# Performance work log

Measured on AMD Instinct MI355X. Metric: run time of the kernel, lower is better.

The kernel has to match this reference:

```python
import jax, jax.numpy as jnp
import numpy as np

EMBED_DIM = 1024
NUM_HEADS = 16
HEAD_DIM = EMBED_DIM // NUM_HEADS


def setup_inputs() -> dict:
    key = jax.random.key(0)
    k_x, k_qkv, k_proj, k_pb = jax.random.split(key, 4)
    B, N = 8, 1024
    s = 1.0 / np.sqrt(EMBED_DIM)
    return {
        "x": jax.random.normal(k_x, (B, N, EMBED_DIM), dtype=jnp.float32),
        # qkv: Linear(embed_dim -> 3*all_head_dim), bias=False
        "w_qkv": jax.random.uniform(k_qkv, (EMBED_DIM, 3 * EMBED_DIM), dtype=jnp.float32, minval=-s, maxval=s),
        # proj: Linear(all_head_dim -> embed_dim), with bias
        "w_proj": jax.random.uniform(k_proj, (EMBED_DIM, EMBED_DIM), dtype=jnp.float32, minval=-s, maxval=s),
        "b_proj": jax.random.uniform(k_pb, (EMBED_DIM,), dtype=jnp.float32, minval=-s, maxval=s),
    }


def reference(x, w_qkv, w_proj, b_proj):
    B, N, _ = x.shape
    scale = HEAD_DIM ** -0.5
    qkv = jnp.einsum("bnd,de->bne", x, w_qkv)  # [B, N, 3*D]
    q, k, v = jnp.split(qkv, 3, axis=-1)
    # reshape to heads: [B, H, N, hd]
    def heads(t):
        return t.reshape(B, N, NUM_HEADS, HEAD_DIM).transpose(0, 2, 1, 3)
    q, k, v = heads(q), heads(k), heads(v)
    attn = jnp.einsum("bhqd,bhkd->bhqk", q, k) * scale
    attn = jax.nn.softmax(attn, axis=-1)
    out = jnp.einsum("bhqk,bhkd->bhqd", attn, v)
    out = out.transpose(0, 2, 1, 3).reshape(B, N, NUM_HEADS * HEAD_DIM)
    return jnp.einsum("bnd,de->bne", out, w_proj) + b_proj
```

## Files before the change

kernel.cpp:

```cpp
#include <hip/hip_runtime.h>
#include <hip/hip_bf16.h>
#include <stdint.h>

typedef __hip_bfloat16 bf16;
typedef __attribute__((ext_vector_type(8))) __bf16 bf16x8;
typedef __attribute__((ext_vector_type(4))) float f32x4;

__device__ __forceinline__ bf16x8 load8bf(const bf16* p) {
    return __builtin_bit_cast(bf16x8, *(const int4*)p);
}

__device__ __forceinline__ void async16(const bf16* g, bf16* l) {
    __builtin_amdgcn_global_load_lds((const __attribute__((address_space(1))) void*)g,
                                     (__attribute__((address_space(3))) void*)l, 16, 0, 0);
}

__global__ __launch_bounds__(256) void cast_x_kernel(const float* __restrict__ in,
                                                     bf16* __restrict__ out, int n4) {
    int i = blockIdx.x * 256 + threadIdx.x;
    if (i >= n4) return;
    float4 v = ((const float4*)in)[i];
    ushort4 o;
    o.x = __builtin_bit_cast(unsigned short, __float2bfloat16(v.x));
    o.y = __builtin_bit_cast(unsigned short, __float2bfloat16(v.y));
    o.z = __builtin_bit_cast(unsigned short, __float2bfloat16(v.z));
    o.w = __builtin_bit_cast(unsigned short, __float2bfloat16(v.w));
    ((ushort4*)out)[i] = o;
}

__global__ __launch_bounds__(256) void transpose_cast(const float* __restrict__ in,
                                                      bf16* __restrict__ out, int R, int C) {
    __shared__ float t[32][33];
    int c0 = blockIdx.x * 32, r0 = blockIdx.y * 32;
    int tx = threadIdx.x, ty = threadIdx.y;
#pragma unroll
    for (int j = 0; j < 32; j += 8)
        t[ty + j][tx] = in[(size_t)(r0 + ty + j) * C + c0 + tx];
    __syncthreads();
#pragma unroll
    for (int j = 0; j < 32; j += 8)
        out[(size_t)(c0 + ty + j) * R + r0 + tx] = __float2bfloat16(t[tx][ty + j]);
}

template <int MODE>
__global__ __launch_bounds__(256) void gemm_bt(
    const bf16* __restrict__ A, const bf16* __restrict__ Bt,
    int M, int N, int K,
    bf16* __restrict__ qo, bf16* __restrict__ ko, bf16* __restrict__ vto,
    float* __restrict__ out, const float* __restrict__ bias) {
    __shared__ __align__(16) bf16 Al0[128 * 64];
    __shared__ __align__(16) bf16 Bl0[128 * 64];
    __shared__ __align__(16) bf16 Al1[128 * 64];
    __shared__ __align__(16) bf16 Bl1[128 * 64];
    const int tid = threadIdx.x;
    const int l = tid & 63, wid = tid >> 6;
    const int lo = l & 15, hi = l >> 4;
    const int wm = wid >> 1, wn = wid & 1;
    const int m0 = blockIdx.x * 128, n0 = blockIdx.y * 128;
    const int sr = tid >> 3;
    const int cl = (tid & 7) * 8;
    const int csw = ((tid & 7) ^ (sr & 7)) * 8;

    f32x4 acc[4][4];
#pragma unroll
    for (int i = 0; i < 4; ++i)
#pragma unroll
        for (int j = 0; j < 4; ++j) acc[i][j] = f32x4{0.f, 0.f, 0.f, 0.f};

#define STAGE_A(DST, KT)                                                              \
    _Pragma("unroll") for (int s_ = 0; s_ < 4; ++s_) {                                \
        int r_ = s_ * 32 + sr;                                                        \
        async16(A + (size_t)(m0 + r_) * K + (KT) * 64 + csw, DST + r_ * 64 + cl);     \
    }
#define STAGE_B(DST, KT)                                                              \
    _Pragma("unroll") for (int s_ = 0; s_ < 4; ++s_) {                                \
        int r_ = s_ * 32 + sr;                                                        \
        async16(Bt + (size_t)(n0 + r_) * K + (KT) * 64 + csw, DST + r_ * 64 + cl);    \
    }
#define KBODY(AL, BL, ANXT, BNXT, KT, STG)                                            \
    {                                                                                 \
        __syncthreads();        \
        if (STG) { STAGE_A(ANXT, (KT) + 1); }                                         \
        __builtin_amdgcn_sched_barrier(0);                                            \
        bf16x8 af[4][2], bfv0[2][2];                                                  \
        _Pragma("unroll") for (int mt = 0; mt < 4; ++mt) {                            \
            int ar = wm * 64 + mt * 16 + lo;                                          \
            _Pragma("unroll") for (int ks = 0; ks < 2; ++ks)                          \
                af[mt][ks] = load8bf(AL + ar * 64 + ((ks * 32 + hi * 8) ^ ((ar & 7) * 8))); \
        }                                                                             \
        _Pragma("unroll") for (int nt = 0; nt < 2; ++nt) {                            \
            int br = wn * 64 + nt * 16 + lo;                                          \
            _Pragma("unroll") for (int ks = 0; ks < 2; ++ks)                          \
                bfv0[nt][ks] = load8bf(BL + br * 64 + ((ks * 32 + hi * 8) ^ ((br & 7) * 8))); \
        }                                                                             \
        _Pragma("unroll") for (int mt = 0; mt < 4; ++mt)                              \
            _Pragma("unroll") for (int nt = 0; nt < 2; ++nt)                          \
                _Pragma("unroll") for (int ks = 0; ks < 2; ++ks)                      \
                    acc[mt][nt] = __builtin_amdgcn_mfma_f32_16x16x32_bf16(            \
                        af[mt][ks], bfv0[nt][ks], acc[mt][nt], 0, 0, 0);              \
        if (STG) { STAGE_B(BNXT, (KT) + 1); }                                         \
        __builtin_amdgcn_sched_barrier(0);                                            \
        bf16x8 bfv1[2][2];                                                            \
        _Pragma("unroll") for (int nt = 0; nt < 2; ++nt) {                            \
            int br = wn * 64 + (nt + 2) * 16 + lo;                                    \
            _Pragma("unroll") for (int ks = 0; ks < 2; ++ks)                          \
                bfv1[nt][ks] = load8bf(BL + br * 64 + ((ks * 32 + hi * 8) ^ ((br & 7) * 8))); \
        }                                                                             \
        _Pragma("unroll") for (int mt = 0; mt < 4; ++mt)                              \
            _Pragma("unroll") for (int nt = 0; nt < 2; ++nt)                          \
                _Pragma("unroll") for (int ks = 0; ks < 2; ++ks)                      \
                    acc[mt][nt + 2] = __builtin_amdgcn_mfma_f32_16x16x32_bf16(        \
                        af[mt][ks], bfv1[nt][ks], acc[mt][nt + 2], 0, 0, 0);          \
    }

    const int nkt = K / 64;
    STAGE_A(Al0, 0)
    STAGE_B(Bl0, 0)
    for (int kt = 0; kt < nkt; kt += 2) {
        KBODY(Al0, Bl0, Al1, Bl1, kt, true)
        KBODY(Al1, Bl1, Al0, Bl0, kt + 1, (kt + 2 < nkt))
    }
#undef KBODY
#undef STAGE_B
#undef STAGE_A

#pragma unroll
    for (int mt = 0; mt < 4; ++mt)
#pragma unroll
        for (int nt = 0; nt < 4; ++nt)
#pragma unroll
            for (int r = 0; r < 4; ++r) {
                int row = m0 + wm * 64 + mt * 16 + hi * 4 + r;
                int col = n0 + wn * 64 + nt * 16 + lo;
                float v = acc[mt][nt][r];
                if (MODE == 0) {
                    if (col < 1024) {
                        qo[(size_t)row * 1024 + col] = __float2bfloat16(v * 0.125f);
                    } else if (col < 2048) {
                        ko[(size_t)row * 1024 + (col - 1024)] = __float2bfloat16(v);
                    } else {
                        int c = col - 2048;
                        vto[((size_t)(row >> 10) * 1024 + c) * 1024 + (row & 1023)] = __float2bfloat16(v);
                    }
                } else {
                    out[(size_t)row * N + col] = v + bias[col];
                }
            }
}

__global__ __launch_bounds__(256, 3) void flash_attn(
    const bf16* __restrict__ q,
    const bf16* __restrict__ kin,
    const bf16* __restrict__ vt,
    bf16* __restrict__ out)
{
    __shared__ __align__(16) bf16 Kl0[64 * 64];
    __shared__ __align__(16) bf16 Vl0[64 * 64];
    __shared__ __align__(16) bf16 Kl1[64 * 64];
    __shared__ __align__(16) bf16 Vl1[64 * 64];
    __shared__ __align__(16) bf16 Pl[4 * 32 * 72];
    const int tid = threadIdx.x;
    const int l = tid & 63, w = tid >> 6;
    const int lo = l & 15, hi = l >> 4;
    const int bid = (blockIdx.x & 7) * 128 + (blockIdx.x >> 3);
    const int qt = bid & 7, h = (bid >> 3) & 15, b = bid >> 7;
    const int ts_r = tid >> 3;
    const int ts_c = tid & 7;
    const int ts_csw = (ts_c ^ (ts_r & 7)) * 8;
    const int ts_lds = tid * 8;

    const bf16* kbase = kin + (size_t)(b * 1024) * 1024 + h * 64;
    const bf16* vbase = vt + (size_t)(b * 1024 + h * 64) * 1024;

#define STAGE_KV(KD, VD, KT)                                                          \
    {                                                                                 \
        async16(kbase + (size_t)((KT) * 64 + ts_r) * 1024 + ts_csw, (KD) + ts_lds);   \
        async16(kbase + (size_t)((KT) * 64 + 32 + ts_r) * 1024 + ts_csw,              \
                (KD) + 2048 + ts_lds);                                                \
        async16(vbase + (size_t)ts_r * 1024 + (KT) * 64 + ts_csw, (VD) + ts_lds);     \
        async16(vbase + (size_t)(32 + ts_r) * 1024 + (KT) * 64 + ts_csw,              \
                (VD) + 2048 + ts_lds);                                                \
    }

    bf16x8 qf[2][2];
#pragma unroll
    for (int mt = 0; mt < 2; ++mt)
#pragma unroll
        for (int ks = 0; ks < 2; ++ks) {
            int tok = qt * 128 + w * 32 + mt * 16 + lo;
            qf[mt][ks] = load8bf(q + (size_t)(b * 1024 + tok) * 1024 + h * 64 + ks * 32 + hi * 8);
        }

    float lsum[2][4];
    f32x4 oacc[2][4];
#pragma unroll
    for (int mt = 0; mt < 2; ++mt)
#pragma unroll
        for (int r = 0; r < 4; ++r) lsum[mt][r] = 0.f;
#pragma unroll
    for (int mt = 0; mt < 2; ++mt)
#pragma unroll
        for (int nt = 0; nt < 4; ++nt) oacc[mt][nt] = f32x4{0.f, 0.f, 0.f, 0.f};

    STAGE_KV(Kl0, Vl0, 0)
    __syncthreads();

#define FA_ITER(KC, VC, KN, VN, KT, STG)                                              \
    {                                                                                 \
        if (STG) { STAGE_KV(KN, VN, (KT) + 1) }                                       \
        __builtin_amdgcn_sched_barrier(0);                                            \
        f32x4 s[2][4];                                                                \
        _Pragma("unroll") for (int mt = 0; mt < 2; ++mt)                              \
            _Pragma("unroll") for (int nt = 0; nt < 4; ++nt)                          \
                s[mt][nt] = f32x4{0.f, 0.f, 0.f, 0.f};                                \
        _Pragma("unroll") for (int ks = 0; ks < 2; ++ks) {                            \
            bf16x8 kf[4];                                                             \
            _Pragma("unroll") for (int nt = 0; nt < 4; ++nt) {                        \
                int kr = nt * 16 + lo;                                                \
                kf[nt] = load8bf((KC) + kr * 64 + ((ks * 32 + hi * 8) ^ ((kr & 7) * 8))); \
            }                                                                         \
            _Pragma("unroll") for (int mt = 0; mt < 2; ++mt)                          \
                _Pragma("unroll") for (int nt = 0; nt < 4; ++nt)                      \
                    s[mt][nt] = __builtin_amdgcn_mfma_f32_16x16x32_bf16(              \
                        qf[mt][ks], kf[nt], s[mt][nt], 0, 0, 0);                      \
        }                                                                             \
        _Pragma("unroll") for (int mt = 0; mt < 2; ++mt)                              \
            _Pragma("unroll") for (int nt = 0; nt < 4; ++nt)                          \
                _Pragma("unroll") for (int r = 0; r < 4; ++r) {                       \
                    float p = __expf(s[mt][nt][r]);                                   \
                    lsum[mt][r] += p;                                                 \
                    Pl[(w * 32 + mt * 16 + hi * 4 + r) * 72 + nt * 16 + lo] =         \
                        __float2bfloat16(p);                                          \
                }                                                                     \
        _Pragma("unroll") for (int ks = 0; ks < 2; ++ks) {                            \
            bf16x8 vf[4], pf[2];                                                      \
            _Pragma("unroll") for (int nt = 0; nt < 4; ++nt) {                        \
                int vr = nt * 16 + lo;                                                \
                vf[nt] = load8bf((VC) + vr * 64 + ((ks * 32 + hi * 8) ^ ((vr & 7) * 8))); \
            }                                                                         \
            _Pragma("unroll") for (int mt = 0; mt < 2; ++mt)                          \
                pf[mt] = load8bf(Pl + (w * 32 + mt * 16 + lo) * 72 + ks * 32 + hi * 8); \
            _Pragma("unroll") for (int mt = 0; mt < 2; ++mt)                          \
                _Pragma("unroll") for (int nt = 0; nt < 4; ++nt)                      \
                    oacc[mt][nt] = __builtin_amdgcn_mfma_f32_16x16x32_bf16(           \
                        pf[mt], vf[nt], oacc[mt][nt], 0, 0, 0);                       \
        }                                                                             \
        __syncthreads();        \
    }

    for (int kt = 0; kt < 16; kt += 2) {
        FA_ITER(Kl0, Vl0, Kl1, Vl1, kt, true)
        FA_ITER(Kl1, Vl1, Kl0, Vl0, kt + 1, (kt + 2 < 16))
    }
#undef FA_ITER
#undef STAGE_KV

#pragma unroll
    for (int mt = 0; mt < 2; ++mt)
#pragma unroll
        for (int r = 0; r < 4; ++r) {
#pragma unroll
            for (int off = 1; off < 16; off <<= 1)
                lsum[mt][r] += __shfl_xor(lsum[mt][r], off);
        }

#pragma unroll
    for (int mt = 0; mt < 2; ++mt)
#pragma unroll
        for (int nt = 0; nt < 4; ++nt)
#pragma unroll
            for (int r = 0; r < 4; ++r) {
                int tok = qt * 128 + w * 32 + mt * 16 + hi * 4 + r;
                int d = nt * 16 + lo;
                out[(size_t)(b * 1024 + tok) * 1024 + h * 64 + d] =
                    __float2bfloat16(oacc[mt][nt][r] / lsum[mt][r]);
            }
}

extern "C" void kernel_launch(void* const* d_in, const int* in_sizes, int n_in,
                              void* d_out, int out_size, void* d_ws, size_t ws_size,
                              hipStream_t stream) {
    const float* x      = (const float*)d_in[0];
    const float* w_qkv  = (const float*)d_in[1];
    const float* w_proj = (const float*)d_in[2];
    const float* b_proj = (const float*)d_in[3];
    float* out = (float*)d_out;

    char* ws = (char*)d_ws;
    bf16* xb     = (bf16*)(ws);
    bf16* wqkvT  = (bf16*)(ws + (16ull << 20));
    bf16* wprojT = (bf16*)(ws + (22ull << 20));
    bf16* qb     = (bf16*)(ws + (24ull << 20));
    bf16* kb     = (bf16*)(ws + (40ull << 20));
    bf16* vtb    = (bf16*)(ws + (56ull << 20));
    bf16* attn   = xb;

    cast_x_kernel<<<8192, 256, 0, stream>>>(x, xb, 2 * 1024 * 1024);
    transpose_cast<<<dim3(96, 32), dim3(32, 8), 0, stream>>>(w_qkv, wqkvT, 1024, 3072);
    transpose_cast<<<dim3(32, 32), dim3(32, 8), 0, stream>>>(w_proj, wprojT, 1024, 1024);
    gemm_bt<0><<<dim3(64, 24), 256, 0, stream>>>(xb, wqkvT, 8192, 3072, 1024,
                                                 qb, kb, vtb, nullptr, nullptr);
    flash_attn<<<1024, 256, 0, stream>>>(qb, kb, vtb, attn);
    gemm_bt<1><<<dim3(64, 8), 256, 0, stream>>>(attn, wprojT, 8192, 1024, 1024,
                                                nullptr, nullptr, nullptr, out, b_proj);
}
```

Measured before the change: 157.1 us.

## Triple-buffer GEMM K-loop with 32-wide tiles and explicit vmcnt waits

The GEMM mainloop moves from double-buffered 64-wide K tiles to triple-buffered 32-wide K tiles, prefetching two stages ahead. Each iteration is fenced with raw s_barrier and explicit s_waitcnt vmcnt counts, so loads can stay in flight across iterations. Shared memory per block is smaller and the kernel requests 3 blocks per CU through launch bounds, aiming for more latency hiding and higher occupancy. The tail is hard-coded for K/32 = 32 iterations, so the kernel is only correct for K=1024, and the hand-written waitcnt values have to match exactly how many async loads are outstanding.

```diff
diff --git a/kernel.cpp b/kernel.cpp
--- a/kernel.cpp
+++ b/kernel.cpp
@@ -43,23 +43,27 @@
 }
 
 template <int MODE>
-__global__ __launch_bounds__(256) void gemm_bt(
+__global__ __launch_bounds__(256, 3) void gemm_bt(
     const bf16* __restrict__ A, const bf16* __restrict__ Bt,
     int M, int N, int K,
     bf16* __restrict__ qo, bf16* __restrict__ ko, bf16* __restrict__ vto,
     float* __restrict__ out, const float* __restrict__ bias) {
-    __shared__ __align__(16) bf16 Al0[128 * 64];
-    __shared__ __align__(16) bf16 Bl0[128 * 64];
-    __shared__ __align__(16) bf16 Al1[128 * 64];
-    __shared__ __align__(16) bf16 Bl1[128 * 64];
+    __shared__ __align__(16) bf16 A0[128 * 32];
+    __shared__ __align__(16) bf16 B0[128 * 32];
+    __shared__ __align__(16) bf16 A1[128 * 32];
+    __shared__ __align__(16) bf16 B1[128 * 32];
+    __shared__ __align__(16) bf16 A2[128 * 32];
+    __shared__ __align__(16) bf16 B2[128 * 32];
     const int tid = threadIdx.x;
     const int l = tid & 63, wid = tid >> 6;
     const int lo = l & 15, hi = l >> 4;
     const int wm = wid >> 1, wn = wid & 1;
     const int m0 = blockIdx.x * 128, n0 = blockIdx.y * 128;
-    const int sr = tid >> 3;
-    const int cl = (tid & 7) * 8;
-    const int csw = ((tid & 7) ^ (sr & 7)) * 8;
+    const int tsr = tid >> 2;
+    const int tsc = tid & 3;
+    const int csw = ((tsc ^ (tsr & 3)) * 8);
+    const int cl  = tsc * 8;
+    const int colr = ((hi ^ (lo & 3)) * 8);
 
     f32x4 acc[4][4];
 #pragma unroll
@@ -67,62 +71,51 @@
 #pragma unroll
         for (int j = 0; j < 4; ++j) acc[i][j] = f32x4{0.f, 0.f, 0.f, 0.f};
 
-#define STAGE_A(DST, KT)                                                              \
-    _Pragma("unroll") for (int s_ = 0; s_ < 4; ++s_) {                                \
-        int r_ = s_ * 32 + sr;                                                        \
-        async16(A + (size_t)(m0 + r_) * K + (KT) * 64 + csw, DST + r_ * 64 + cl);     \
-    }
-#define STAGE_B(DST, KT)                                                              \
-    _Pragma("unroll") for (int s_ = 0; s_ < 4; ++s_) {                                \
-        int r_ = s_ * 32 + sr;                                                        \
-        async16(Bt + (size_t)(n0 + r_) * K + (KT) * 64 + csw, DST + r_ * 64 + cl);    \
-    }
-#define KBODY(AL, BL, ANXT, BNXT, KT, STG)                                            \
-    {                                                                                 \
-        __syncthreads();        \
-        if (STG) { STAGE_A(ANXT, (KT) + 1); }                                         \
-        __builtin_amdgcn_sched_barrier(0);                                            \
-        bf16x8 af[4][2], bfv0[2][2];                                                  \
-        _Pragma("unroll") for (int mt = 0; mt < 4; ++mt) {                            \
-            int ar = wm * 64 + mt * 16 + lo;                                          \
-            _Pragma("unroll") for (int ks = 0; ks < 2; ++ks)                          \
-                af[mt][ks] = load8bf(AL + ar * 64 + ((ks * 32 + hi * 8) ^ ((ar & 7) * 8))); \
-        }                                                                             \
-        _Pragma("unroll") for (int nt = 0; nt < 2; ++nt) {                            \
-            int br = wn * 64 + nt * 16 + lo;                                          \
-            _Pragma("unroll") for (int ks = 0; ks < 2; ++ks)                          \
-                bfv0[nt][ks] = load8bf(BL + br * 64 + ((ks * 32 + hi * 8) ^ ((br & 7) * 8))); \
-        }                                                                             \
+#define STAGE32(AD, BD, KT)                                                           \
+    {                                                                                 \
+        async16(A + (size_t)(m0 + tsr) * K + (KT) * 32 + csw, (AD) + tsr * 32 + cl);  \
+        async16(A + (size_t)(m0 + 64 + tsr) * K + (KT) * 32 + csw,                    \
+                (AD) + (64 + tsr) * 32 + cl);                                         \
+        async16(Bt + (size_t)(n0 + tsr) * K + (KT) * 32 + csw, (BD) + tsr * 32 + cl); \
+        async16(Bt + (size_t)(n0 + 64 + tsr) * K + (KT) * 32 + csw,                   \
+                (BD) + (64 + tsr) * 32 + cl);                                         \
+    }
+
+#define KB(AC, BC, AS, BS, KT, STG, WAITASM)                                          \
+    {                                                                                 \
+        __builtin_amdgcn_s_barrier();           \
+        __builtin_amdgcn_sched_barrier(0);       \
+        if (STG) STAGE32(AS, BS, (KT) + 2)                                            \
+        __builtin_amdgcn_sched_barrier(0);          \
+        asm volatile(WAITASM ::: "memory");                                           \
+        __builtin_amdgcn_s_barrier();            \
+        __builtin_amdgcn_sched_barrier(0);       \
+        bf16x8 af[4], bf_[4];                                                         \
         _Pragma("unroll") for (int mt = 0; mt < 4; ++mt)                              \
-            _Pragma("unroll") for (int nt = 0; nt < 2; ++nt)                          \
-                _Pragma("unroll") for (int ks = 0; ks < 2; ++ks)                      \
-                    acc[mt][nt] = __builtin_amdgcn_mfma_f32_16x16x32_bf16(            \
-                        af[mt][ks], bfv0[nt][ks], acc[mt][nt], 0, 0, 0);              \
-        if (STG) { STAGE_B(BNXT, (KT) + 1); }                                         \
-        __builtin_amdgcn_sched_barrier(0);                                            \
-        bf16x8 bfv1[2][2];                                                            \
-        _Pragma("unroll") for (int nt = 0; nt < 2; ++nt) {                            \
-            int br = wn * 64 + (nt + 2) * 16 + lo;                                    \
-            _Pragma("unroll") for (int ks = 0; ks < 2; ++ks)                          \
-                bfv1[nt][ks] = load8bf(BL + br * 64 + ((ks * 32 + hi * 8) ^ ((br & 7) * 8))); \
-        }                                                                             \
+            af[mt] = load8bf((AC) + (wm * 64 + mt * 16 + lo) * 32 + colr);            \
+        _Pragma("unroll") for (int nt = 0; nt < 4; ++nt)                              \
+            bf_[nt] = load8bf((BC) + (wn * 64 + nt * 16 + lo) * 32 + colr);           \
         _Pragma("unroll") for (int mt = 0; mt < 4; ++mt)                              \
-            _Pragma("unroll") for (int nt = 0; nt < 2; ++nt)                          \
-                _Pragma("unroll") for (int ks = 0; ks < 2; ++ks)                      \
-                    acc[mt][nt + 2] = __builtin_amdgcn_mfma_f32_16x16x32_bf16(        \
-                        af[mt][ks], bfv1[nt][ks], acc[mt][nt + 2], 0, 0, 0);          \
-    }
-
-    const int nkt = K / 64;
-    STAGE_A(Al0, 0)
-    STAGE_B(Bl0, 0)
-    for (int kt = 0; kt < nkt; kt += 2) {
-        KBODY(Al0, Bl0, Al1, Bl1, kt, true)
-        KBODY(Al1, Bl1, Al0, Bl0, kt + 1, (kt + 2 < nkt))
-    }
-#undef KBODY
-#undef STAGE_B
-#undef STAGE_A
+            _Pragma("unroll") for (int nt = 0; nt < 4; ++nt)                          \
+                acc[mt][nt] = __builtin_amdgcn_mfma_f32_16x16x32_bf16(                \
+                    af[mt], bf_[nt], acc[mt][nt], 0, 0, 0);                           \
+    }
+
+    const int nkt = K / 32;
+    STAGE32(A0, B0, 0)
+    STAGE32(A1, B1, 1)
+    for (int kt = 0; kt + 5 < nkt; kt += 3) {
+        KB(A0, B0, A2, B2, kt, true, "s_waitcnt vmcnt(8)")
+        KB(A1, B1, A0, B0, kt + 1, true, "s_waitcnt vmcnt(8)")
+        KB(A2, B2, A1, B1, kt + 2, true, "s_waitcnt vmcnt(8)")
+    }
+    KB(A0, B0, A2, B2, 27, true, "s_waitcnt vmcnt(8)")
+    KB(A1, B1, A0, B0, 28, true, "s_waitcnt vmcnt(8)")
+    KB(A2, B2, A1, B1, 29, true, "s_waitcnt vmcnt(8)")
+    KB(A0, B0, A2, B2, 30, false, "s_waitcnt vmcnt(4)")
+    KB(A1, B1, A2, B2, 31, false, "s_waitcnt vmcnt(0)")
+#undef KB
+#undef STAGE32
 
 #pragma unroll
     for (int mt = 0; mt < 4; ++mt)
@@ -245,7 +238,7 @@
                     oacc[mt][nt] = __builtin_amdgcn_mfma_f32_16x16x32_bf16(           \
                         pf[mt], vf[nt], oacc[mt][nt], 0, 0, 0);                       \
         }                                                                             \
-        __syncthreads();        \
+        __syncthreads();                                                              \
     }
 
     for (int kt = 0; kt < 16; kt += 2) {
```

New measurement: 166.0 us. +5.6%, slower.
